# Performance work log

Hardware: AMD Instinct MI355X
Metric: run time of the kernel (lower is better)

## Reference

```python
import jax, jax.numpy as jnp
import numpy as np

B, L, D, H = 2, 2048, 1024, 16
HD = D // H
SCALE = HD ** (-0.5)


def setup_inputs() -> dict:
    key = jax.random.key(0)
    ks = jax.random.split(key, 12)
    mk = lambda k, shape: (0.02 * jax.random.normal(k, shape, dtype=jnp.float32))
    return {
        "x_real": jax.random.normal(ks[0], (B, L, D), dtype=jnp.float32),
        "x_imag": jax.random.normal(ks[1], (B, L, D), dtype=jnp.float32),
        "wq_r": mk(ks[2], (D, D)),
        "wq_i": mk(ks[3], (D, D)),
        "wk_r": mk(ks[4], (D, D)),
        "wk_i": mk(ks[5], (D, D)),
        "wv_r": mk(ks[6], (D, D)),
        "wv_i": mk(ks[7], (D, D)),
        "wo_r": mk(ks[8], (D, D)),
        "wo_i": mk(ks[9], (D, D)),
        "bo_r": jnp.zeros((D,), dtype=jnp.float32),
        "bo_i": jnp.zeros((D,), dtype=jnp.float32),
    }


def _clinear(xr, xi, wr, wi):
    # (a+bi)(c+di): real = a@Wr^T - b@Wi^T ; imag = a@Wi^T + b@Wr^T
    r = xr @ wr.T - xi @ wi.T
    i = xr @ wi.T + xi @ wr.T
    return r, i


def _heads(t):
    # [B,L,D] -> [B,H,L,hd]
    return t.reshape(B, L, H, HD).transpose(0, 2, 1, 3)


def reference(x_real, x_imag, wq_r, wq_i, wk_r, wk_i, wv_r, wv_i, wo_r, wo_i, bo_r, bo_i):
    Qr, Qi = _clinear(x_real, x_imag, wq_r, wq_i)
    Kr, Ki = _clinear(x_real, x_imag, wk_r, wk_i)
    Vr, Vi = _clinear(x_real, x_imag, wv_r, wv_i)
    Qr, Qi, Kr, Ki, Vr, Vi = map(_heads, (Qr, Qi, Kr, Ki, Vr, Vi))

    # real part of complex dot product: Re(Q)Re(K)^T + Im(Q)Im(K)^T
    scores = (jnp.einsum("bhqd,bhkd->bhqk", Qr, Kr)
              + jnp.einsum("bhqd,bhkd->bhqk", Qi, Ki)) * SCALE
    causal = jnp.tril(jnp.ones((L, L), dtype=bool))
    scores = jnp.where(causal, scores, -jnp.inf)
    w = jax.nn.softmax(scores, axis=-1)

    out_r = jnp.einsum("bhqk,bhkd->bhqd", w, Vr)
    out_i = jnp.einsum("bhqk,bhkd->bhqd", w, Vi)
    merge = lambda t: t.transpose(0, 2, 1, 3).reshape(B, L, D)
    out_r, out_i = merge(out_r), merge(out_i)

    yr, yi = _clinear(out_r, out_i, wo_r, wo_i)
    return yr + bo_r, yi + bo_i
```

## Files before the change

### kernel.cpp

```cpp
#include <hip/hip_runtime.h>
#include <hip/hip_bf16.h>


using f32x4  = __attribute__((ext_vector_type(4))) float;
using short8 = __attribute__((ext_vector_type(8))) short;
using bf16_t = __hip_bfloat16;

#define AS1 __attribute__((address_space(1)))
#define AS3 __attribute__((address_space(3)))

__device__ __forceinline__ void gload_lds16(const bf16_t* g, bf16_t* l) {
  __builtin_amdgcn_global_load_lds((const AS1 unsigned int*)g, (AS3 unsigned int*)l, 16, 0, 0);
}

__device__ __forceinline__ unsigned short bfbits(float f) {
  union { bf16_t h; unsigned short u; } c; c.h = __float2bfloat16(f); return c.u;
}

__global__ void pack_x_k(const float* __restrict__ xr, const float* __restrict__ xi,
                         bf16_t* __restrict__ out) {
  const int total4 = 4096 * 2048 / 4;
  for (int idx = blockIdx.x * blockDim.x + threadIdx.x; idx < total4;
       idx += gridDim.x * blockDim.x) {
    int m = idx >> 9, k = (idx & 511) * 4;
    const float* src = (k < 1024) ? (xr + (size_t)m * 1024 + k)
                                  : (xi + (size_t)m * 1024 + (k - 1024));
    float4 v = *(const float4*)src;
    unsigned int lo = (unsigned)bfbits(v.x) | ((unsigned)bfbits(v.y) << 16);
    unsigned int hi = (unsigned)bfbits(v.z) | ((unsigned)bfbits(v.w) << 16);
    *(uint2*)(out + (size_t)idx * 4) = make_uint2(lo, hi);
  }
}

__global__ void pack_wqkv_k(const float* __restrict__ wqr, const float* __restrict__ wqi,
                            const float* __restrict__ wkr, const float* __restrict__ wki,
                            const float* __restrict__ wvr, const float* __restrict__ wvi,
                            bf16_t* __restrict__ out) {
  const int total4 = 6144 * 2048 / 4;
  for (int idx = blockIdx.x * blockDim.x + threadIdx.x; idx < total4;
       idx += gridDim.x * blockDim.x) {
    int row = idx >> 9, k = (idx & 511) * 4;
    int sec = row >> 10, r1 = row & 1023;
    bool lowk = (k < 1024);
    int kk = lowk ? k : (k - 1024);
    const float* base = wqr; float sg = 1.f;
    switch (sec) {
      case 0: base = lowk ? wqr : wqi; sg = lowk ? 1.f : -1.f; break;
      case 1: base = lowk ? wqi : wqr; break;
      case 2: base = lowk ? wkr : wki; sg = lowk ? 1.f : -1.f; break;
      case 3: base = lowk ? wki : wkr; break;
      case 4: base = lowk ? wvr : wvi; sg = lowk ? 1.f : -1.f; break;
      case 5: base = lowk ? wvi : wvr; break;
    }
    float4 v = *(const float4*)(base + (size_t)r1 * 1024 + kk);
    unsigned int lo = (unsigned)bfbits(v.x * sg) | ((unsigned)bfbits(v.y * sg) << 16);
    unsigned int hi = (unsigned)bfbits(v.z * sg) | ((unsigned)bfbits(v.w * sg) << 16);
    *(uint2*)(out + (size_t)idx * 4) = make_uint2(lo, hi);
  }
}

__global__ void pack_wo_k(const float* __restrict__ wor, const float* __restrict__ woi,
                          bf16_t* __restrict__ out) {
  const int total4 = 2048 * 2048 / 4;
  for (int idx = blockIdx.x * blockDim.x + threadIdx.x; idx < total4;
       idx += gridDim.x * blockDim.x) {
    int row = idx >> 9, k = (idx & 511) * 4;
    int sec = row >> 10, r1 = row & 1023;
    bool lowk = (k < 1024);
    int kk = lowk ? k : (k - 1024);
    const float* base; float sg = 1.f;
    if (sec == 0) { base = lowk ? wor : woi; sg = lowk ? 1.f : -1.f; }
    else          { base = lowk ? woi : wor; }
    float4 v = *(const float4*)(base + (size_t)r1 * 1024 + kk);
    unsigned int lo = (unsigned)bfbits(v.x * sg) | ((unsigned)bfbits(v.y * sg) << 16);
    unsigned int hi = (unsigned)bfbits(v.z * sg) | ((unsigned)bfbits(v.w * sg) << 16);
    *(uint2*)(out + (size_t)idx * 4) = make_uint2(lo, hi);
  }
}

__device__ __forceinline__ void gemm_core(const bf16_t* __restrict__ A,
                                          const bf16_t* __restrict__ W,
                                          int m0, int n0, f32x4 (&acc)[4][4]) {
  __shared__ __align__(16) bf16_t sA[128 * 64];
  __shared__ __align__(16) bf16_t sB[128 * 64];
  const int tid = threadIdx.x;
  const int lane = tid & 63, w = tid >> 6;
  const int wr = w >> 1, wc = w & 1;
  const int quad = lane >> 4, m16 = lane & 15;
  const int srow = w * 32 + (lane >> 3);
  const int gcol = (((lane & 7) ^ (lane >> 3)) * 8);
  const int swz7 = m16 & 7;
  for (int k0 = 0; k0 < 2048; k0 += 64) {
    __syncthreads();
#pragma unroll
    for (int i = 0; i < 4; ++i) {
      gload_lds16(A + (size_t)(m0 + srow + i * 8) * 2048 + k0 + gcol,
                  sA + (size_t)(w * 32 + i * 8) * 64 + lane * 8);
      gload_lds16(W + (size_t)(n0 + srow + i * 8) * 2048 + k0 + gcol,
                  sB + (size_t)(w * 32 + i * 8) * 64 + lane * 8);
    }
    __syncthreads();
#pragma unroll
    for (int kk = 0; kk < 2; ++kk) {
      short8 af[4], bf[4];
#pragma unroll
      for (int i = 0; i < 4; ++i)
        af[i] = *(const short8*)(sA + (wr * 64 + i * 16 + m16) * 64 +
                                 ((kk * 4 + quad) ^ swz7) * 8);
#pragma unroll
      for (int j = 0; j < 4; ++j)
        bf[j] = *(const short8*)(sB + (wc * 64 + j * 16 + m16) * 64 +
                                 ((kk * 4 + quad) ^ swz7) * 8);
#pragma unroll
      for (int i = 0; i < 4; ++i)
#pragma unroll
        for (int j = 0; j < 4; ++j)
          acc[i][j] = __builtin_amdgcn_mfma_f32_16x16x32_bf16(af[i], bf[j], acc[i][j], 0, 0, 0);
    }
  }
}

__global__ __launch_bounds__(512, 2) void gemm_qkv_k(const bf16_t* __restrict__ A,
                                                     const bf16_t* __restrict__ W,
                                                     bf16_t* __restrict__ qk,
                                                     bf16_t* __restrict__ vt) {
  __shared__ __align__(16) bf16_t sA[2][256 * 64];
  __shared__ __align__(16) bf16_t sB[2][192 * 64];
  const int tid = threadIdx.x, lane = tid & 63, w = tid >> 6;
  const int wm = w >> 2, wn = w & 3;
  const int quad = lane >> 4, m16 = lane & 15;
  const int swz7 = m16 & 7;
  const int m0 = blockIdx.x * 256, n0 = blockIdx.y * 192;
  const int NT = 32;

  const int l3 = lane >> 3;
  const int gcol = (((lane & 7) ^ l3) * 8);

  f32x4 acc[8][3] = {};

  auto stageA = [&](int buf, int half, int k0) {
#pragma unroll
    for (int i = 0; i < 2; ++i)
      gload_lds16(A + (size_t)(m0 + half * 128 + w * 16 + i * 8 + l3) * 2048 + k0 + gcol,
                  &sA[buf][(size_t)(half * 128 + w * 16 + i * 8) * 64] + lane * 8);
  };
  auto stageB = [&](int buf, int c, int k0) {
    gload_lds16(W + (size_t)(n0 + c * 64 + w * 8 + l3) * 2048 + k0 + gcol,
                &sB[buf][(size_t)(c * 64 + w * 8) * 64] + lane * 8);
  };

  stageA(0, 0, 0); stageA(0, 1, 0);
  stageB(0, 0, 0); stageB(0, 1, 0); stageB(0, 2, 0);
  stageB(1, 0, 64); stageB(1, 1, 64); stageB(1, 2, 64);
  asm volatile("s_waitcnt vmcnt(3)" ::: "memory");
  __builtin_amdgcn_s_barrier();

  for (int t = 0; t < NT; ++t) {
    const int p = t & 1, q = p ^ 1;
    const bf16_t* sAp = sA[p];
    const bf16_t* sBp = sB[p];
    short8 af[4], bfr[3];
#pragma unroll
    for (int ph = 0; ph < 4; ++ph) {
      const int kk = ph >> 1, mh = ph & 1;
#pragma unroll
      for (int i = 0; i < 4; ++i)
        af[i] = *(const short8*)(sAp + (wm * 128 + (mh * 4 + i) * 16 + m16) * 64 +
                                 ((kk * 4 + quad) ^ swz7) * 8);
      if (mh == 0) {
#pragma unroll
        for (int j = 0; j < 3; ++j)
          bfr[j] = *(const short8*)(sBp + (wn * 48 + j * 16 + m16) * 64 +
                                    ((kk * 4 + quad) ^ swz7) * 8);
      }
      if (ph == 0)      { if (t + 1 < NT) stageA(q, 0, (t + 1) * 64); }
      else if (ph == 1) { if (t + 1 < NT) stageA(q, 1, (t + 1) * 64); }
      else if (ph == 3) {
        if (t + 2 < NT) {
          stageB(p, 0, (t + 2) * 64); stageB(p, 1, (t + 2) * 64); stageB(p, 2, (t + 2) * 64);
        }
      }
      asm volatile("" ::: "memory");
      __builtin_amdgcn_s_barrier();
      __builtin_amdgcn_s_setprio(1);
#pragma unroll
      for (int i = 0; i < 4; ++i)
#pragma unroll
        for (int j = 0; j < 3; ++j)
          acc[mh * 4 + i][j] = __builtin_amdgcn_mfma_f32_16x16x32_bf16(af[i], bfr[j],
                                                                       acc[mh * 4 + i][j], 0, 0, 0);
      __builtin_amdgcn_s_setprio(0);
      asm volatile("" ::: "memory");
      if (ph == 3) {
        if (t == NT - 2)      asm volatile("s_waitcnt vmcnt(0)" ::: "memory");
        else if (t < NT - 2)  asm volatile("s_waitcnt vmcnt(3)" ::: "memory");
      }
      __builtin_amdgcn_s_barrier();
    }
  }

#pragma unroll
  for (int mf = 0; mf < 8; ++mf) {
    const int rowb = m0 + wm * 128 + mf * 16 + quad * 4;
#pragma unroll
    for (int nf = 0; nf < 3; ++nf) {
      const int col = n0 + wn * 48 + nf * 16 + m16;
      if (col < 4096) {
        const float sc = (col < 2048) ? 0.125f : 1.f;
#pragma unroll
        for (int r = 0; r < 4; ++r)
          qk[(size_t)(rowb + r) * 4096 + col] = __float2bfloat16(acc[mf][nf][r] * sc);
      } else {
        const int vcol = col - 4096;
        const int ri = vcol >> 10, dfeat = vcol & 1023;
        const int b = rowb >> 11, seq = rowb & 2047;
        const size_t vrow = (size_t)(b * 2048 + (dfeat >> 6) * 128 + ri * 64 + (dfeat & 63));
        unsigned int lo = (unsigned)bfbits(acc[mf][nf][0]) | ((unsigned)bfbits(acc[mf][nf][1]) << 16);
        unsigned int hi = (unsigned)bfbits(acc[mf][nf][2]) | ((unsigned)bfbits(acc[mf][nf][3]) << 16);
        *(uint2*)(vt + vrow * 2048 + seq) = make_uint2(lo, hi);
      }
    }
  }
}

__global__ __launch_bounds__(256) void gemm_out_k(const bf16_t* __restrict__ A,
                                                  const bf16_t* __restrict__ W,
                                                  const float* __restrict__ bor,
                                                  const float* __restrict__ boi,
                                                  float* __restrict__ out) {
  f32x4 acc[4][4] = {};
  const int m0 = blockIdx.x * 128, n0 = blockIdx.y * 128;
  gemm_core(A, W, m0, n0, acc);
  const int lane = threadIdx.x & 63, w = threadIdx.x >> 6;
  const int wr = w >> 1, wc = w & 1, quad = lane >> 4, m16 = lane & 15;
#pragma unroll
  for (int i = 0; i < 4; ++i) {
    const int rowb = m0 + wr * 64 + i * 16 + quad * 4;
#pragma unroll
    for (int j = 0; j < 4; ++j) {
      const int col = n0 + wc * 64 + j * 16 + m16;
      float bias; float* op;
      if (col < 1024) { bias = bor[col]; op = out + col; }
      else            { bias = boi[col - 1024]; op = out + 4194304 + (col - 1024); }
#pragma unroll
      for (int r = 0; r < 4; ++r)
        op[(size_t)(rowb + r) * 1024] = acc[i][j][r] + bias;
    }
  }
}

__global__ __launch_bounds__(512, 4) void attn_k(const bf16_t* __restrict__ qk,
                                                 const bf16_t* __restrict__ vt,
                                                 bf16_t* __restrict__ acat) {
  __shared__ __align__(16) bf16_t sK[64 * 128];
  __shared__ __align__(16) bf16_t sV[144 * 64];
  __shared__ __align__(16) bf16_t sP[8][16 * 72];
  const int tid = threadIdx.x, lane = tid & 63, w = tid >> 6;
  const int wq = w & 3, sub = w >> 2;
  const int quad = lane >> 4, m16 = lane & 15;
  const int x = blockIdx.x, bh = blockIdx.y, b = bh >> 4, h = bh & 15;
  const size_t qkrow0 = (size_t)b * 2048;
  const int qA = x * 64, qB = (31 - x) * 64;
  const int nT = 32 - x;
  const int swz7 = m16 & 7;
  const int qbase = (sub ? qB : qA) + wq * 16;

  if (tid < 256) {
    const int rr = tid >> 4, cb = (tid & 15) * 4;
    const bf16_t v = __float2bfloat16(rr == 0 ? 1.f : 0.f);
#pragma unroll
    for (int i = 0; i < 4; ++i) sV[(128 + rr) * 64 + cb + i] = v;
  }

  short8 qf[4];
  {
    const bf16_t* qa = qk + (qkrow0 + qbase + m16) * 4096;
#pragma unroll
    for (int kk = 0; kk < 4; ++kk) {
      const int col = (kk >> 1) * 1024 + h * 64 + (kk & 1) * 32 + quad * 8;
      qf[kk] = *(const short8*)(qa + col);
    }
  }
  f32x4 o[9];
#pragma unroll
  for (int j = 0; j < 9; ++j) o[j] = (f32x4){0.f, 0.f, 0.f, 0.f};

  const int qrow = qbase + quad * 4;

  const int kl4 = lane >> 4, kl15 = lane & 15;
  const int vl3 = lane >> 3;
  const int vg7 = ((lane & 7) ^ vl3) * 8;

  for (int t = 0; t < nT; ++t) {
    const int k0 = t * 64;
    __syncthreads();
#pragma unroll
    for (int i = 0; i < 2; ++i) {
      const int row = w * 8 + i * 4 + kl4;
      const int g = kl15 ^ (row & 7);
      const int col = 2048 + (g >> 3) * 1024 + h * 64 + (g & 7) * 8;
      gload_lds16(qk + (qkrow0 + k0 + row) * 4096 + col,
                  sK + (size_t)(w * 8 + i * 4) * 128 + lane * 8);
    }
#pragma unroll
    for (int i = 0; i < 2; ++i) {
      const int row = w * 16 + i * 8 + vl3;
      gload_lds16(vt + ((size_t)bh * 128 + row) * 2048 + k0 + vg7,
                  sV + (size_t)(w * 16 + i * 8) * 64 + lane * 8);
    }
    __syncthreads();

    const bool act = sub ? true : (t <= x);
    if (act) {
      const bool dg = sub ? (t == nT - 1) : (t == x);

      f32x4 sv[4];
#pragma unroll
      for (int jt = 0; jt < 4; ++jt) {
        f32x4 a = (f32x4){0.f, 0.f, 0.f, 0.f};
#pragma unroll
        for (int kk = 0; kk < 4; ++kk) {
          short8 kf = *(const short8*)(sK + (jt * 16 + m16) * 128 +
                                       ((kk * 4 + quad) ^ swz7) * 8);
          a = __builtin_amdgcn_mfma_f32_16x16x32_bf16(qf[kk], kf, a, 0, 0, 0);
        }
        sv[jt] = a;
      }

      bf16_t* pw = sP[w];
#pragma unroll
      for (int jt = 0; jt < 4; ++jt)
#pragma unroll
        for (int r = 0; r < 4; ++r) {
          float s = sv[jt][r];
          if (dg && (k0 + jt * 16 + m16 > qrow + r)) s = -1e30f;
          pw[(quad * 4 + r) * 72 + jt * 16 + m16] = __float2bfloat16(__expf(s));
        }
      asm volatile("s_waitcnt lgkmcnt(0)" ::: "memory");

#pragma unroll
      for (int kc = 0; kc < 2; ++kc) {
        short8 p = *(const short8*)(pw + m16 * 72 + kc * 32 + quad * 8);
#pragma unroll
        for (int j = 0; j < 9; ++j) {
          short8 vf = *(const short8*)(sV + (j * 16 + m16) * 64 +
                                       ((kc * 4 + quad) ^ swz7) * 8);
          o[j] = __builtin_amdgcn_mfma_f32_16x16x32_bf16(p, vf, o[j], 0, 0, 0);
        }
      }
    }
  }

  float inv[4];
#pragma unroll
  for (int r = 0; r < 4; ++r)
    inv[r] = 1.f / __shfl(o[8][r], lane & 48);
#pragma unroll
  for (int j = 0; j < 8; ++j) {
    const int d = j * 16 + m16;
    const int col = (d < 64) ? (h * 64 + d) : (1024 + h * 64 + (d - 64));
#pragma unroll
    for (int r = 0; r < 4; ++r)
      acat[((size_t)b * 2048 + qrow + r) * 2048 + col] = __float2bfloat16(o[j][r] * inv[r]);
  }
}

extern "C" void kernel_launch(void* const* d_in, const int* in_sizes, int n_in,
                              void* d_out, int out_size, void* d_ws, size_t ws_size,
                              hipStream_t stream) {
  const float* xr  = (const float*)d_in[0];
  const float* xi  = (const float*)d_in[1];
  const float* wqr = (const float*)d_in[2];
  const float* wqi = (const float*)d_in[3];
  const float* wkr = (const float*)d_in[4];
  const float* wki = (const float*)d_in[5];
  const float* wvr = (const float*)d_in[6];
  const float* wvi = (const float*)d_in[7];
  const float* wor = (const float*)d_in[8];
  const float* woi = (const float*)d_in[9];
  const float* bor = (const float*)d_in[10];
  const float* boi = (const float*)d_in[11];
  float* out = (float*)d_out;

  char* ws = (char*)d_ws;
  bf16_t* Xcat = (bf16_t*)(ws);
  bf16_t* Wqkv = (bf16_t*)(ws + 16777216ull);
  bf16_t* QKb  = (bf16_t*)(ws + 41943040ull);
  bf16_t* Vt   = (bf16_t*)(ws + 75497472ull);
  bf16_t* Acat = (bf16_t*)(ws + 92274688ull);
  bf16_t* Wo   = (bf16_t*)(ws + 109051904ull);

  pack_x_k<<<2048, 256, 0, stream>>>(xr, xi, Xcat);
  pack_wqkv_k<<<2048, 256, 0, stream>>>(wqr, wqi, wkr, wki, wvr, wvi, Wqkv);
  pack_wo_k<<<1024, 256, 0, stream>>>(wor, woi, Wo);
  gemm_qkv_k<<<dim3(16, 32), 512, 0, stream>>>(Xcat, Wqkv, QKb, Vt);
  attn_k<<<dim3(16, 32), 512, 0, stream>>>(QKb, Vt, Acat);
  gemm_out_k<<<dim3(32, 16), 256, 0, stream>>>(Acat, Wo, bor, boi, out);
}
```

Measured before the change: 356.8 us.

## Software-pipeline QKV GEMM main loop with register-prefetched fragments and one barrier

Restructures the bf16 MFMA main loop of the QKV projection GEMM. LDS fragments for the next sub-step are read into spare registers (A0/A1, B0/B1) while the current MFMA group runs, and the four per-phase barriers per K-tile drop to a single barrier. The goal is to hide LDS read latency and cut synchronisation stalls. In exchange it uses more registers, waits for all outstanding global loads (vmcnt(0)) each tile, and redundantly restages the A tile for buffer 1 in the prologue.

```diff
diff --git a/kernel.cpp b/kernel.cpp
--- a/kernel.cpp
+++ b/kernel.cpp
@@ -148,55 +148,89 @@
     gload_lds16(W + (size_t)(n0 + c * 64 + w * 8 + l3) * 2048 + k0 + gcol,
                 &sB[buf][(size_t)(c * 64 + w * 8) * 64] + lane * 8);
   };
+  auto rdA = [&](const bf16_t* sAx, int mf, int kk) -> short8 {
+    return *(const short8*)(sAx + (wm * 128 + mf * 16 + m16) * 64 +
+                            ((kk * 4 + quad) ^ swz7) * 8);
+  };
+  auto rdB = [&](const bf16_t* sBx, int j, int kk) -> short8 {
+    return *(const short8*)(sBx + (wn * 48 + j * 16 + m16) * 64 +
+                            ((kk * 4 + quad) ^ swz7) * 8);
+  };
 
   stageA(0, 0, 0); stageA(0, 1, 0);
   stageB(0, 0, 0); stageB(0, 1, 0); stageB(0, 2, 0);
+  stageA(1, 0, 64); stageA(1, 1, 64);
   stageB(1, 0, 64); stageB(1, 1, 64); stageB(1, 2, 64);
-  asm volatile("s_waitcnt vmcnt(3)" ::: "memory");
+  asm volatile("s_waitcnt vmcnt(7)" ::: "memory");
   __builtin_amdgcn_s_barrier();
+
+  short8 A0[4], A1[4], B0[3], B1[3];
+#pragma unroll
+  for (int i = 0; i < 4; ++i) A0[i] = rdA(sA[0], i, 0);
+#pragma unroll
+  for (int j = 0; j < 3; ++j) B0[j] = rdB(sB[0], j, 0);
 
   for (int t = 0; t < NT; ++t) {
     const int p = t & 1, q = p ^ 1;
     const bf16_t* sAp = sA[p];
     const bf16_t* sBp = sB[p];
-    short8 af[4], bfr[3];
-#pragma unroll
-    for (int ph = 0; ph < 4; ++ph) {
-      const int kk = ph >> 1, mh = ph & 1;
-#pragma unroll
-      for (int i = 0; i < 4; ++i)
-        af[i] = *(const short8*)(sAp + (wm * 128 + (mh * 4 + i) * 16 + m16) * 64 +
-                                 ((kk * 4 + quad) ^ swz7) * 8);
-      if (mh == 0) {
-#pragma unroll
-        for (int j = 0; j < 3; ++j)
-          bfr[j] = *(const short8*)(sBp + (wn * 48 + j * 16 + m16) * 64 +
-                                    ((kk * 4 + quad) ^ swz7) * 8);
-      }
-      if (ph == 0)      { if (t + 1 < NT) stageA(q, 0, (t + 1) * 64); }
-      else if (ph == 1) { if (t + 1 < NT) stageA(q, 1, (t + 1) * 64); }
-      else if (ph == 3) {
-        if (t + 2 < NT) {
-          stageB(p, 0, (t + 2) * 64); stageB(p, 1, (t + 2) * 64); stageB(p, 2, (t + 2) * 64);
-        }
-      }
-      asm volatile("" ::: "memory");
-      __builtin_amdgcn_s_barrier();
-      __builtin_amdgcn_s_setprio(1);
-#pragma unroll
-      for (int i = 0; i < 4; ++i)
-#pragma unroll
-        for (int j = 0; j < 3; ++j)
-          acc[mh * 4 + i][j] = __builtin_amdgcn_mfma_f32_16x16x32_bf16(af[i], bfr[j],
-                                                                       acc[mh * 4 + i][j], 0, 0, 0);
-      __builtin_amdgcn_s_setprio(0);
-      asm volatile("" ::: "memory");
-      if (ph == 3) {
-        if (t == NT - 2)      asm volatile("s_waitcnt vmcnt(0)" ::: "memory");
-        else if (t < NT - 2)  asm volatile("s_waitcnt vmcnt(3)" ::: "memory");
-      }
-      __builtin_amdgcn_s_barrier();
-    }
+    const bf16_t* sAq = sA[q];
+    const bf16_t* sBq = sB[q];
+    const bool stg = (t + 1 < NT);
+
+#pragma unroll
+    for (int i = 0; i < 4; ++i) A1[i] = rdA(sAp, 4 + i, 0);
+    if (stg) stageA(q, 0, (t + 1) * 64);
+    __builtin_amdgcn_s_setprio(1);
+#pragma unroll
+    for (int i = 0; i < 4; ++i)
+#pragma unroll
+      for (int j = 0; j < 3; ++j)
+        acc[i][j] = __builtin_amdgcn_mfma_f32_16x16x32_bf16(A0[i], B0[j], acc[i][j], 0, 0, 0);
+    __builtin_amdgcn_s_setprio(0);
+
+#pragma unroll
+    for (int i = 0; i < 4; ++i) A0[i] = rdA(sAp, i, 1);
+#pragma unroll
+    for (int j = 0; j < 3; ++j) B1[j] = rdB(sBp, j, 1);
+    if (stg) stageA(q, 1, (t + 1) * 64);
+    __builtin_amdgcn_s_setprio(1);
+#pragma unroll
+    for (int i = 0; i < 4; ++i)
+#pragma unroll
+      for (int j = 0; j < 3; ++j)
+        acc[4 + i][j] = __builtin_amdgcn_mfma_f32_16x16x32_bf16(A1[i], B0[j], acc[4 + i][j], 0, 0, 0);
+    __builtin_amdgcn_s_setprio(0);
+
+#pragma unroll
+    for (int i = 0; i < 4; ++i) A1[i] = rdA(sAp, 4 + i, 1);
+    __builtin_amdgcn_s_setprio(1);
+#pragma unroll
+    for (int i = 0; i < 4; ++i)
+#pragma unroll
+      for (int j = 0; j < 3; ++j)
+        acc[i][j] = __builtin_amdgcn_mfma_f32_16x16x32_bf16(A0[i], B1[j], acc[i][j], 0, 0, 0);
+    __builtin_amdgcn_s_setprio(0);
+
+    asm volatile("s_waitcnt vmcnt(0)" ::: "memory");
+    __builtin_amdgcn_s_barrier();
+
+    if (stg) {
+#pragma unroll
+      for (int i = 0; i < 4; ++i) A0[i] = rdA(sAq, i, 0);
+#pragma unroll
+      for (int j = 0; j < 3; ++j) B0[j] = rdB(sBq, j, 0);
+    }
+    if (t + 2 < NT) {
+      stageB(p, 0, (t + 2) * 64); stageB(p, 1, (t + 2) * 64); stageB(p, 2, (t + 2) * 64);
+    }
+    __builtin_amdgcn_s_setprio(1);
+#pragma unroll
+    for (int i = 0; i < 4; ++i)
+#pragma unroll
+      for (int j = 0; j < 3; ++j)
+        acc[4 + i][j] = __builtin_amdgcn_mfma_f32_16x16x32_bf16(A1[i], B1[j], acc[4 + i][j], 0, 0, 0);
+    __builtin_amdgcn_s_setprio(0);
   }
 
 #pragma unroll
```

After: 352.3 us. No clear change (-1.3%).
